# Kernel optimization log

Measured on AMD Instinct MI355X. Metric: run time of the kernel, lower is better.

## Reference

```python
import jax, jax.numpy as jnp
import numpy as np

NUM_CLASSES = 20
NUM_ANCHORS = 3
STRIDES = (8, 16, 32)
FMP = (320, 160, 80)
TOPK = 100
CONF_THRESH = 0.01
NMS_THRESH = 0.5
ANCHOR_SIZE = np.array([[12, 16], [19, 36], [40, 28], [36, 75], [76, 55], [72, 146],
                        [142, 110], [192, 243], [459, 401]], dtype=np.float32).reshape(3, NUM_ANCHORS, 2)


def make_anchors(level):
    h = w = FMP[level]
    ys, xs = jnp.meshgrid(jnp.arange(h, dtype=jnp.float32), jnp.arange(w, dtype=jnp.float32), indexing='ij')
    xy = jnp.stack([xs, ys], axis=-1).reshape(-1, 1, 2) + 0.5            # [HW,1,2] grid centers
    xy = jnp.broadcast_to(xy, (h * w, NUM_ANCHORS, 2))
    wh = jnp.broadcast_to(jnp.asarray(ANCHOR_SIZE[level]), (h * w, NUM_ANCHORS, 2))
    return jnp.concatenate([xy, wh], axis=-1).reshape(-1, 4)             # [HW*A, 4]


def level_topk(obj, cls, reg, level):
    C = NUM_CLASSES
    # [1, ch, H, W] -> [H*W*A, ch_per_anchor], matching permute(1,2,0).view(-1, .)
    obj = obj[0].transpose(1, 2, 0).reshape(-1, 1)
    cls = cls[0].transpose(1, 2, 0).reshape(-1, C)
    reg = reg[0].transpose(1, 2, 0).reshape(-1, 4)
    anchors = make_anchors(level)
    # decode: ctr = (sigmoid(txy)*3 - 1.5 + grid) * stride ; wh = exp(twh) * anchor_wh
    ctr = (jax.nn.sigmoid(reg[:, :2]) * 3.0 - 1.5 + anchors[:, :2]) * STRIDES[level]
    wh = jnp.exp(reg[:, 2:]) * anchors[:, 2:]
    boxes = jnp.concatenate([ctr - 0.5 * wh, ctr + 0.5 * wh], axis=-1)   # [N, 4] xyxy
    scores = (jax.nn.sigmoid(obj) * jax.nn.sigmoid(cls)).reshape(-1)     # [N*C]
    top_s, top_i = jax.lax.top_k(scores, TOPK)
    anchor_idx = top_i // C
    labels = top_i % C
    return top_s, labels, boxes[anchor_idx], top_s > CONF_THRESH


def nms_fixed(boxes, scores, labels, valid):
    # class-aware greedy NMS on a fixed candidate set; suppressed entries get score 0 / keep False
    K = scores.shape[0]
    order = jnp.argsort(-scores)
    b, s, l, v = boxes[order], scores[order], labels[order], valid[order]
    areas = (b[:, 2] - b[:, 0]) * (b[:, 3] - b[:, 1])
    xx1 = jnp.maximum(b[:, None, 0], b[None, :, 0])
    yy1 = jnp.maximum(b[:, None, 1], b[None, :, 1])
    xx2 = jnp.minimum(b[:, None, 2], b[None, :, 2])
    yy2 = jnp.minimum(b[:, None, 3], b[None, :, 3])
    inter = jnp.maximum(1e-10, xx2 - xx1) * jnp.maximum(1e-10, yy2 - yy1)
    iou = inter / (areas[:, None] + areas[None, :] - inter)
    sup_mat = (iou > NMS_THRESH) & (l[:, None] == l[None, :])            # per-class suppression
    idx = jnp.arange(K)

    def body(i, state):
        suppressed, keep = state
        is_kept = jnp.logical_and(jnp.logical_not(suppressed[i]), v[i])
        keep = keep.at[i].set(is_kept)
        suppressed = suppressed | (is_kept & sup_mat[i] & (idx > i))
        return suppressed, keep

    _, keep = jax.lax.fori_loop(0, K, body, (jnp.zeros(K, bool), jnp.zeros(K, bool)))
    return b, s * keep.astype(s.dtype), l, keep


def setup_inputs() -> dict:
    key = jax.random.key(0)
    ks = jax.random.split(key, 9)
    shapes = {
        'obj0': (1, NUM_ANCHORS, 320, 320), 'cls0': (1, NUM_ANCHORS * NUM_CLASSES, 320, 320), 'reg0': (1, NUM_ANCHORS * 4, 320, 320),
        'obj1': (1, NUM_ANCHORS, 160, 160), 'cls1': (1, NUM_ANCHORS * NUM_CLASSES, 160, 160), 'reg1': (1, NUM_ANCHORS * 4, 160, 160),
        'obj2': (1, NUM_ANCHORS, 80, 80), 'cls2': (1, NUM_ANCHORS * NUM_CLASSES, 80, 80), 'reg2': (1, NUM_ANCHORS * 4, 80, 80),
    }
    return {name: jax.random.normal(k, shp, dtype=jnp.float32)
            for k, (name, shp) in zip(ks, shapes.items())}


def reference(obj0, cls0, reg0, obj1, cls1, reg1, obj2, cls2, reg2):
    levels = [(obj0, cls0, reg0), (obj1, cls1, reg1), (obj2, cls2, reg2)]
    parts = [level_topk(o, c, r, i) for i, (o, c, r) in enumerate(levels)]
    scores = jnp.concatenate([p[0] for p in parts])
    labels = jnp.concatenate([p[1] for p in parts])
    boxes = jnp.concatenate([p[2] for p in parts])
    valid = jnp.concatenate([p[3] for p in parts])
    return nms_fixed(boxes, scores, labels, valid)  # (bboxes[300,4], scores[300], labels[300], keep[300])
```

## Files before the change

kernel.cpp:

```cpp
#include <hip/hip_runtime.h>
#include <stdint.h>

typedef unsigned int u32;
typedef unsigned long long u64;

#define TOPK 100
#define CAP 4096
#define NB 512
#define BINBASE 32000u
#define KAB_BLOCKS 788

__device__ const float ANC[3][3][2] = {
  {{12.f,16.f},{19.f,36.f},{40.f,28.f}},
  {{36.f,75.f},{76.f,55.f},{72.f,146.f}},
  {{142.f,110.f},{192.f,243.f},{459.f,401.f}}
};

__device__ __forceinline__ float sigmoidf_(float x) {
  if (x >= 0.f) return 1.f / (1.f + expf(-x));
  float e = expf(x);
  return e / (1.f + e);
}

__device__ __forceinline__ float fcomp2(const float2& v, int q) {
  return q ? v.y : v.x;
}

__global__ __launch_bounds__(256) void kA_scan(
    const float* __restrict__ obj0, const float* __restrict__ cls0,
    const float* __restrict__ obj1, const float* __restrict__ cls1,
    const float* __restrict__ obj2, const float* __restrict__ cls2,
    u32* __restrict__ hist, float* __restrict__ amax)
{
  __shared__ u32 h[NB];
  int tid = threadIdx.x;
  h[tid] = 0; h[tid + 256] = 0;
  __syncthreads();

  int b = blockIdx.x;
  const float *obj, *cls; int P, L, abase; u32 task;
  if (b < 600)      { L=0; obj=obj0; cls=cls0; P=102400; abase=0;      task=(u32)(b*256+tid); }
  else if (b < 750) { L=1; obj=obj1; cls=cls1; P=25600;  abase=307200; task=(u32)((b-600)*256+tid); }
  else              { L=2; obj=obj2; cls=cls2; P=6400;   abase=384000; task=(u32)((b-750)*256+tid); }
  int tpa = P >> 1;
  bool valid = task < (u32)(3*tpa);

  if (valid) {
    int a = (int)(task / (u32)tpa), rem = (int)(task % (u32)tpa);
    int p0 = rem * 2;
    float2 o2 = *(const float2*)(obj + a*P + p0);
    const float* cp = cls + (size_t)(a*20)*P + p0;
    float2 cv[20];
    #pragma unroll
    for (int k = 0; k < 20; ++k) cv[k] = *(const float2*)(cp + (size_t)k*P);
    float2 cm = cv[0];
    #pragma unroll
    for (int k = 1; k < 20; ++k) {
      cm.x = fmaxf(cm.x, cv[k].x); cm.y = fmaxf(cm.y, cv[k].y);
    }
    float2 am2;
    am2.x = sigmoidf_(o2.x) * sigmoidf_(cm.x);
    am2.y = sigmoidf_(o2.y) * sigmoidf_(cm.y);
    *(float2*)(amax + abase + a*P + p0) = am2;
    #pragma unroll
    for (int q = 0; q < 2; ++q) {
      u32 bt = __float_as_uint(fcomp2(am2, q));
      if (bt >= (BINBASE << 15)) {
        u32 bin = (bt >> 15) - BINBASE;
        if (bin < NB) atomicAdd(&h[bin], 1u);
      }
    }
  }
  __syncthreads();
  if (h[tid])       atomicAdd(&hist[L*NB + tid],       h[tid]);
  if (h[tid + 256]) atomicAdd(&hist[L*NB + tid + 256], h[tid + 256]);
}

__global__ __launch_bounds__(256) void kB_collect(
    const float* __restrict__ obj0, const float* __restrict__ cls0,
    const float* __restrict__ obj1, const float* __restrict__ cls1,
    const float* __restrict__ obj2, const float* __restrict__ cls2,
    const float* __restrict__ amax, const u32* __restrict__ hist,
    u32* __restrict__ cnt, u64* __restrict__ cand)
{
  __shared__ u32 s[NB];
  __shared__ u32 sThr;
  int tid = threadIdx.x;
  int b = blockIdx.x;
  const float *obj, *cls; int P, L, abase; u32 task;
  if (b < 600)      { L=0; obj=obj0; cls=cls0; P=102400; abase=0;      task=(u32)(b*256+tid); }
  else if (b < 750) { L=1; obj=obj1; cls=cls1; P=25600;  abase=307200; task=(u32)((b-600)*256+tid); }
  else              { L=2; obj=obj2; cls=cls2; P=6400;   abase=384000; task=(u32)((b-750)*256+tid); }
  int tpa = P >> 1;
  bool valid = task < (u32)(3*tpa);

  s[tid] = hist[L*NB + tid]; s[tid + 256] = hist[L*NB + tid + 256];
  __syncthreads();
  for (int off = 1; off < NB; off <<= 1) {
    u32 v0 = s[tid]       + ((tid + off < NB)       ? s[tid + off]       : 0u);
    u32 v1 = s[tid + 256] + ((tid + 256 + off < NB) ? s[tid + 256 + off] : 0u);
    __syncthreads();
    s[tid] = v0; s[tid + 256] = v1;
    __syncthreads();
  }
  if (tid == 0 && s[0] < TOPK) sThr = BINBASE << 15;
  {
    int i0 = tid, i1 = tid + 256;
    u32 a0 = s[i0], n0 = (i0 + 1 < NB) ? s[i0 + 1] : 0u;
    if (a0 >= TOPK && n0 < TOPK) sThr = (BINBASE + (u32)i0) << 15;
    u32 a1 = s[i1], n1 = (i1 + 1 < NB) ? s[i1 + 1] : 0u;
    if (a1 >= TOPK && n1 < TOPK) sThr = (BINBASE + (u32)i1) << 15;
  }
  __syncthreads();
  u32 thr = sThr;

  if (valid) {
    int a = (int)(task / (u32)tpa), rem = (int)(task % (u32)tpa);
    int p0 = rem * 2;
    float2 am2 = *(const float2*)(amax + abase + a*P + p0);
    bool any = (__float_as_uint(am2.x) >= thr) | (__float_as_uint(am2.y) >= thr);
    if (any) {
      float2 o2 = *(const float2*)(obj + a*P + p0);
      const float* cp = cls + (size_t)(a*20)*P + p0;
      float2 cv[20];
      #pragma unroll
      for (int k = 0; k < 20; ++k) cv[k] = *(const float2*)(cp + (size_t)k*P);
      #pragma unroll
      for (int q = 0; q < 2; ++q) {
        if (__float_as_uint(fcomp2(am2, q)) >= thr) {
          float so = sigmoidf_(fcomp2(o2, q));
          int p = p0 + q;
          #pragma unroll
          for (int k = 0; k < 20; ++k) {
            float sc = so * sigmoidf_(fcomp2(cv[k], q));
            u32 bits = __float_as_uint(sc);
            if (bits >= thr) {
              u32 pos = atomicAdd(&cnt[L], 1u);
              u32 idx = (u32)(p*60 + a*20 + k);
              if (pos < CAP) cand[L*CAP + pos] = ((u64)bits << 32) | (u64)(0x00FFFFFFu - idx);
            }
          }
        }
      }
    }
  }
}

__global__ __launch_bounds__(1024) void kT_select_nms(
    const float* __restrict__ reg0, const float* __restrict__ reg1, const float* __restrict__ reg2,
    const u64* __restrict__ cand, const u32* __restrict__ cnt,
    u64* __restrict__ matg, u32* __restrict__ bar,
    float* __restrict__ out)
{
  extern __shared__ uint8_t smem[];
  u64*    mat   = (u64*)(smem);
  float4* ibox4 = (float4*)(smem + 12000);
  float2* iml2  = (float2*)(smem + 16800);
  float*  x1s   = (float*)(smem + 19200);
  float*  y1s   = (float*)(smem + 20400);
  float*  x2s   = (float*)(smem + 21600);
  float*  y2s   = (float*)(smem + 22800);
  float*  sc2   = (float*)(smem + 24000);
  int*    lb2   = (int*)(smem + 25200);
  int*    vd2   = (int*)(smem + 26400);
  u64*    rowAny= (u64*)(smem + 27600);
  u64*    km    = (u64*)(smem + 27648);
  float*  ars   = (float*)(smem + 27696);
  u64*    sel   = (u64*)(smem + 32800);
  float*  bxs   = (float*)(smem + 35200);
  float*  scs   = (float*)(smem + 40000);
  int*    lbs   = (int*)(smem + 41200);
  int*    vds   = (int*)(smem + 42400);

  int tid = threadIdx.x;
  int b = blockIdx.x;
  if (tid < 300) sel[tid] = 0ull;
  __syncthreads();

  {
    int gL    = (tid >= 768) ? 2 : (tid >= 384) ? 1 : 0;
    int gbase = (gL == 2) ? 768 : (gL == 1) ? 384 : 0;
    int lt    = tid - gbase;
    int gsz   = (gL == 2) ? 256 : 384;

    u32 n = cnt[gL]; if (n > CAP) n = CAP;
    bool useLds = (n <= 496);
    u64* kc = mat + gL*500;
    const u64* cb = cand + gL*CAP;
    u32 n4 = (n + 3u) & ~3u;

    if (useLds) {
      for (u32 j = (u32)lt; j < n; j += gsz) kc[j] = cb[j];
      if (lt < 4 && n + (u32)lt < n4) kc[n + lt] = 0ull;
    }
    __syncthreads();

    if (useLds) {
      for (u32 j = (u32)lt; j < n; j += gsz) {
        u64 kk = kc[j]; int r = 0;
        for (u32 t = 0; t < n4; t += 4) {
          u64 k0 = kc[t], k1 = kc[t+1], k2 = kc[t+2], k3 = kc[t+3];
          r += (k0 > kk) ? 1 : 0; r += (k1 > kk) ? 1 : 0;
          r += (k2 > kk) ? 1 : 0; r += (k3 > kk) ? 1 : 0;
        }
        if (r < TOPK) sel[gL*TOPK + r] = kk;
      }
    } else {
      u32 nn = n & ~3u;
      for (u32 j = (u32)lt; j < n; j += gsz) {
        u64 kk = cb[j]; int r = 0;
        for (u32 t = 0; t < nn; t += 4) {
          r += (cb[t]   > kk) ? 1 : 0; r += (cb[t+1] > kk) ? 1 : 0;
          r += (cb[t+2] > kk) ? 1 : 0; r += (cb[t+3] > kk) ? 1 : 0;
        }
        for (u32 t = nn; t < n; ++t) r += (cb[t] > kk) ? 1 : 0;
        if (r < TOPK) sel[gL*TOPK + r] = kk;
      }
    }
  }
  __syncthreads();

  if (tid < 300) {
    int Lq = tid / TOPK;
    const float* reg; int Pq, W, stride;
    if (Lq == 0)      { reg = reg0; Pq = 102400; W = 320; stride = 8; }
    else if (Lq == 1) { reg = reg1; Pq = 25600;  W = 160; stride = 16; }
    else              { reg = reg2; Pq = 6400;   W = 80;  stride = 32; }
    u64 key = sel[tid];
    if (key == 0) {
      scs[tid] = 0.f; lbs[tid] = 0; vds[tid] = 0;
      bxs[tid*4+0] = bxs[tid*4+1] = bxs[tid*4+2] = bxs[tid*4+3] = 0.f;
    } else {
      float score = __uint_as_float((u32)(key >> 32));
      u32 i = 0x00FFFFFFu - (u32)(key & 0xFFFFFFFFull);
      int c = (int)(i % 60u), p = (int)(i / 60u);
      int aa = c / 20, k = c % 20;
      int x = p % W, y = p / W;
      float tx = reg[(aa*4+0)*Pq + p], ty = reg[(aa*4+1)*Pq + p];
      float tw = reg[(aa*4+2)*Pq + p], th = reg[(aa*4+3)*Pq + p];
      float cx = (sigmoidf_(tx)*3.f - 1.5f + (float)x + 0.5f) * (float)stride;
      float cy = (sigmoidf_(ty)*3.f - 1.5f + (float)y + 0.5f) * (float)stride;
      float bw = expf(tw) * ANC[Lq][aa][0];
      float bh = expf(th) * ANC[Lq][aa][1];
      scs[tid] = score; lbs[tid] = k; vds[tid] = (score > 0.01f) ? 1 : 0;
      bxs[tid*4+0] = cx - 0.5f*bw; bxs[tid*4+1] = cy - 0.5f*bh;
      bxs[tid*4+2] = cx + 0.5f*bw; bxs[tid*4+3] = cy + 0.5f*bh;
    }
  }
  __syncthreads();

  if (tid < 300) {
    int Lm = tid / TOPK, rr = tid % TOPK;
    u64 kk = sel[tid];
    int rank = rr;
    #pragma unroll
    for (int Lo = 0; Lo < 3; ++Lo) {
      if (Lo == Lm) continue;
      const u64* arr = sel + Lo*TOPK;
      bool ge = (Lo < Lm);
      int lo = 0;
      #pragma unroll
      for (int st = 64; st > 0; st >>= 1) {
        int nxt = lo + st;
        if (nxt <= TOPK) {
          u64 v = arr[nxt - 1];
          bool pred = ge ? (v >= kk) : (v > kk);
          if (pred) lo = nxt;
        }
      }
      rank += lo;
    }
    float x1 = bxs[tid*4+0], y1 = bxs[tid*4+1], x2 = bxs[tid*4+2], y2 = bxs[tid*4+3];
    float ar = (x2 - x1) * (y2 - y1);
    ibox4[rank] = make_float4(x1, y1, x2, y2);
    iml2[rank]  = make_float2(ar, (float)lbs[tid]);
    x1s[rank] = x1; y1s[rank] = y1; x2s[rank] = x2; y2s[rank] = y2; ars[rank] = ar;
    sc2[rank] = scs[tid]; lb2[rank] = lbs[tid]; vd2[rank] = vds[tid];
  }
  __syncthreads();

  {
    int w = (b == 0) ? 4 : (b - 1);
    int wave = tid >> 6, lane = tid & 63;
    int j = w*64 + lane;
    bool jv = j < 300;
    float jx1=0.f, jy1=0.f, jx2=0.f, jy2=0.f, jar=0.f; float jlb=-1.f;
    if (jv) { jx1=x1s[j]; jy1=y1s[j]; jx2=x2s[j]; jy2=y2s[j]; jar=ars[j]; jlb=(float)lb2[j]; }
    int ilim = (w+1)*64; if (ilim > 300) ilim = 300;
    for (int i = wave; i < ilim; i += 16) {
      float4 B = ibox4[i];
      float2 M = iml2[i];
      float xx1 = fmaxf(B.x, jx1), yy1 = fmaxf(B.y, jy1);
      float xx2 = fminf(B.z, jx2), yy2 = fminf(B.w, jy2);
      float inter = fmaxf(1e-10f, xx2-xx1) * fmaxf(1e-10f, yy2-yy1);
      float iou = inter / (M.x + jar - inter);
      bool pred = jv && (iou > 0.5f) && (M.y == jlb);
      u64 m = __ballot(pred);
      if (lane == 0) {
        if (b == 0) mat[i*5 + 4] = m;
        else __hip_atomic_store(&matg[i*5 + w], m, __ATOMIC_RELAXED, __HIP_MEMORY_SCOPE_AGENT);
      }
    }
  }
  __syncthreads();

  if (b != 0) {
    if (tid == 0)
      __hip_atomic_fetch_add(bar, 1u, __ATOMIC_RELEASE, __HIP_MEMORY_SCOPE_AGENT);
    return;
  }

  if (tid == 0) {
    while (__hip_atomic_load(bar, __ATOMIC_ACQUIRE, __HIP_MEMORY_SCOPE_AGENT) < 4u)
      __builtin_amdgcn_s_sleep(1);
  }
  __syncthreads();
  for (int idx = tid; idx < 1200; idx += 1024) {
    int w2 = idx / 300, i = idx % 300;
    if (i < (w2+1)*64)
      mat[i*5 + w2] = __hip_atomic_load(&matg[i*5 + w2], __ATOMIC_RELAXED, __HIP_MEMORY_SCOPE_AGENT);
  }
  __syncthreads();

  {
    bool flag = false;
    if (tid < 300) {
      int c = tid >> 6, bq = tid & 63;
      u64 acc = mat[tid*5 + c] & ((bq == 63) ? 0ull : (~0ull << (bq + 1)));
      for (int w = c + 1; w < 5; ++w) acc |= mat[tid*5 + w];
      flag = (acc != 0ull);
    }
    u64 bal = __ballot(flag);
    if ((tid & 63) == 0 && (tid >> 6) < 5) rowAny[tid >> 6] = bal;
  }
  __syncthreads();

  if (tid < 64) {
    int lane = tid;
    u64 vm[5];
    #pragma unroll
    for (int c = 0; c < 5; ++c) {
      int j = c*64 + lane;
      vm[c] = __ballot((j < 300) && (vd2[j] != 0));
    }
    u64 ra[5];
    #pragma unroll
    for (int c = 0; c < 5; ++c) ra[c] = rowAny[c];
    u64 S[5] = {0,0,0,0,0};
    #pragma unroll
    for (int c = 0; c < 5; ++c) {
      u64 kbits = 0;
      int lim = (c == 4) ? 44 : 64;
      for (int t = 0; t < lim; ++t) {
        u64 kept = ((~(S[c] >> t)) & (vm[c] >> t)) & 1ull;
        kbits |= kept << t;
        if (kept & ((ra[c] >> t) & 1ull)) {
          int i = c*64 + t;
          #pragma unroll
          for (int w = 0; w < 5; ++w)
            if (w >= c) S[w] |= mat[i*5 + w];
        }
      }
      if (lane == 0) km[c] = kbits;
    }
  }
  __syncthreads();

  if (tid < 300) {
    float kf = (float)((km[tid >> 6] >> (tid & 63)) & 1ull);
    float4 bq = ibox4[tid];
    out[tid*4+0] = bq.x; out[tid*4+1] = bq.y;
    out[tid*4+2] = bq.z; out[tid*4+3] = bq.w;
    out[1200+tid] = sc2[tid] * kf;
    out[1500+tid] = (float)lb2[tid];
    out[1800+tid] = kf;
  }
}

extern "C" void kernel_launch(void* const* d_in, const int* in_sizes, int n_in,
                              void* d_out, int out_size, void* d_ws, size_t ws_size,
                              hipStream_t stream) {
  const float* obj0 = (const float*)d_in[0];
  const float* cls0 = (const float*)d_in[1];
  const float* reg0 = (const float*)d_in[2];
  const float* obj1 = (const float*)d_in[3];
  const float* cls1 = (const float*)d_in[4];
  const float* reg1 = (const float*)d_in[5];
  const float* obj2 = (const float*)d_in[6];
  const float* cls2 = (const float*)d_in[7];
  const float* reg2 = (const float*)d_in[8];
  float* out = (float*)d_out;

  uint8_t* ws = (uint8_t*)d_ws;
  u32*   hist = (u32*)(ws + 0);
  u32*   cnt  = (u32*)(ws + 6144);
  u32*   bar  = (u32*)(ws + 6156);
  u64*   cand = (u64*)(ws + 8192);
  u64*   matg = (u64*)(ws + 106496);
  float* amax = (float*)(ws + 118496);

  (void)hipMemsetAsync(ws, 0, 6160, stream);

  kA_scan<<<dim3(KAB_BLOCKS), dim3(256), 0, stream>>>(
      obj0, cls0, obj1, cls1, obj2, cls2, hist, amax);
  kB_collect<<<dim3(KAB_BLOCKS), dim3(256), 0, stream>>>(
      obj0, cls0, obj1, cls1, obj2, cls2, amax, hist, cnt, cand);
  kT_select_nms<<<dim3(5), dim3(1024), 43600, stream>>>(
      reg0, reg1, reg2, cand, cnt, matg, bar, out);
}
```

Baseline: 146.2 us.

## Fuse collect and select/NMS kernels via last-blocks-done completion counter

Merges the candidate-collection kernel and the top-k select/NMS kernel into one launch. Blocks are widened to 1024 threads, and a global done counter lets the last five blocks to finish collection take the NMS roles, after spinning until all blocks have arrived. This removes one kernel launch and the inter-kernel gap, but it relies on all blocks being co-resident or finishing so the spin-wait cannot deadlock. It also raises LDS per block to 43.6 KB for every collection block, which may reduce occupancy in the collect phase.

After: 155.7 us. 1.06x slower.

```diff
diff --git a/kernel.cpp b/kernel.cpp
--- a/kernel.cpp
+++ b/kernel.cpp
@@ -8,7 +8,9 @@
 #define CAP 4096
 #define NB 512
 #define BINBASE 32000u
-#define KAB_BLOCKS 788
+#define KA_BLOCKS 788
+#define KBT_BLOCKS 198
+#define FIN_BASE (KBT_BLOCKS - 5)
 
 __device__ const float ANC[3][3][2] = {
   {{12.f,16.f},{19.f,36.f},{40.f,28.f}},
@@ -76,40 +78,62 @@
   if (h[tid + 256]) atomicAdd(&hist[L*NB + tid + 256], h[tid + 256]);
 }
 
-__global__ __launch_bounds__(256) void kB_collect(
+__global__ __launch_bounds__(1024) void kBT_collect_nms(
     const float* __restrict__ obj0, const float* __restrict__ cls0,
     const float* __restrict__ obj1, const float* __restrict__ cls1,
     const float* __restrict__ obj2, const float* __restrict__ cls2,
+    const float* __restrict__ reg0, const float* __restrict__ reg1, const float* __restrict__ reg2,
     const float* __restrict__ amax, const u32* __restrict__ hist,
-    u32* __restrict__ cnt, u64* __restrict__ cand)
+    u32* __restrict__ cnt, u64* __restrict__ cand,
+    u32* __restrict__ done, u32* __restrict__ bar, u64* __restrict__ matg,
+    float* __restrict__ out)
 {
-  __shared__ u32 s[NB];
+  extern __shared__ uint8_t smem[];
+  u32*    s     = (u32*)(smem);
+  u64*    mat   = (u64*)(smem);
+  float4* ibox4 = (float4*)(smem + 12000);
+  float2* iml2  = (float2*)(smem + 16800);
+  float*  x1s   = (float*)(smem + 19200);
+  float*  y1s   = (float*)(smem + 20400);
+  float*  x2s   = (float*)(smem + 21600);
+  float*  y2s   = (float*)(smem + 22800);
+  float*  sc2   = (float*)(smem + 24000);
+  int*    lb2   = (int*)(smem + 25200);
+  int*    vd2   = (int*)(smem + 26400);
+  u64*    rowAny= (u64*)(smem + 27600);
+  u64*    km    = (u64*)(smem + 27648);
+  float*  ars   = (float*)(smem + 27696);
+  u64*    sel   = (u64*)(smem + 32800);
+  float*  bxs   = (float*)(smem + 35200);
+  float*  scs   = (float*)(smem + 40000);
+  int*    lbs   = (int*)(smem + 41200);
+  int*    vds   = (int*)(smem + 42400);
   __shared__ u32 sThr;
+  __shared__ u32 sOld;
+
   int tid = threadIdx.x;
   int b = blockIdx.x;
+
   const float *obj, *cls; int P, L, abase; u32 task;
-  if (b < 600)      { L=0; obj=obj0; cls=cls0; P=102400; abase=0;      task=(u32)(b*256+tid); }
-  else if (b < 750) { L=1; obj=obj1; cls=cls1; P=25600;  abase=307200; task=(u32)((b-600)*256+tid); }
-  else              { L=2; obj=obj2; cls=cls2; P=6400;   abase=384000; task=(u32)((b-750)*256+tid); }
+  if (b < 150)      { L=0; obj=obj0; cls=cls0; P=102400; abase=0;      task=(u32)(b*1024+tid); }
+  else if (b < 188) { L=1; obj=obj1; cls=cls1; P=25600;  abase=307200; task=(u32)((b-150)*1024+tid); }
+  else              { L=2; obj=obj2; cls=cls2; P=6400;   abase=384000; task=(u32)((b-188)*1024+tid); }
   int tpa = P >> 1;
   bool valid = task < (u32)(3*tpa);
 
-  s[tid] = hist[L*NB + tid]; s[tid + 256] = hist[L*NB + tid + 256];
+  if (tid < NB) s[tid] = hist[L*NB + tid];
   __syncthreads();
   for (int off = 1; off < NB; off <<= 1) {
-    u32 v0 = s[tid]       + ((tid + off < NB)       ? s[tid + off]       : 0u);
-    u32 v1 = s[tid + 256] + ((tid + 256 + off < NB) ? s[tid + 256 + off] : 0u);
+    u32 v = 0;
+    if (tid < NB) v = s[tid] + ((tid + off < NB) ? s[tid + off] : 0u);
     __syncthreads();
-    s[tid] = v0; s[tid + 256] = v1;
+    if (tid < NB) s[tid] = v;
     __syncthreads();
   }
   if (tid == 0 && s[0] < TOPK) sThr = BINBASE << 15;
-  {
-    int i0 = tid, i1 = tid + 256;
-    u32 a0 = s[i0], n0 = (i0 + 1 < NB) ? s[i0 + 1] : 0u;
-    if (a0 >= TOPK && n0 < TOPK) sThr = (BINBASE + (u32)i0) << 15;
-    u32 a1 = s[i1], n1 = (i1 + 1 < NB) ? s[i1 + 1] : 0u;
-    if (a1 >= TOPK && n1 < TOPK) sThr = (BINBASE + (u32)i1) << 15;
+  if (tid < NB) {
+    u32 a0 = s[tid], n0 = (tid + 1 < NB) ? s[tid + 1] : 0u;
+    if (a0 >= TOPK && n0 < TOPK) sThr = (BINBASE + (u32)tid) << 15;
   }
   __syncthreads();
   u32 thr = sThr;
@@ -137,43 +161,30 @@
             if (bits >= thr) {
               u32 pos = atomicAdd(&cnt[L], 1u);
               u32 idx = (u32)(p*60 + a*20 + k);
-              if (pos < CAP) cand[L*CAP + pos] = ((u64)bits << 32) | (u64)(0x00FFFFFFu - idx);
+              if (pos < CAP)
+                __hip_atomic_store(&cand[L*CAP + pos],
+                                   ((u64)bits << 32) | (u64)(0x00FFFFFFu - idx),
+                                   __ATOMIC_RELAXED, __HIP_MEMORY_SCOPE_AGENT);
             }
           }
         }
       }
     }
   }
-}
-
-__global__ __launch_bounds__(1024) void kT_select_nms(
-    const float* __restrict__ reg0, const float* __restrict__ reg1, const float* __restrict__ reg2,
-    const u64* __restrict__ cand, const u32* __restrict__ cnt,
-    u64* __restrict__ matg, u32* __restrict__ bar,
-    float* __restrict__ out)
-{
-  extern __shared__ uint8_t smem[];
-  u64*    mat   = (u64*)(smem);
-  float4* ibox4 = (float4*)(smem + 12000);
-  float2* iml2  = (float2*)(smem + 16800);
-  float*  x1s   = (float*)(smem + 19200);
-  float*  y1s   = (float*)(smem + 20400);
-  float*  x2s   = (float*)(smem + 21600);
-  float*  y2s   = (float*)(smem + 22800);
-  float*  sc2   = (float*)(smem + 24000);
-  int*    lb2   = (int*)(smem + 25200);
-  int*    vd2   = (int*)(smem + 26400);
-  u64*    rowAny= (u64*)(smem + 27600);
-  u64*    km    = (u64*)(smem + 27648);
-  float*  ars   = (float*)(smem + 27696);
-  u64*    sel   = (u64*)(smem + 32800);
-  float*  bxs   = (float*)(smem + 35200);
-  float*  scs   = (float*)(smem + 40000);
-  int*    lbs   = (int*)(smem + 41200);
-  int*    vds   = (int*)(smem + 42400);
-
-  int tid = threadIdx.x;
-  int b = blockIdx.x;
+  __syncthreads();
+
+  if (tid == 0) sOld = __hip_atomic_fetch_add(done, 1u, __ATOMIC_ACQ_REL, __HIP_MEMORY_SCOPE_AGENT);
+  __syncthreads();
+  u32 old = sOld;
+  if (old < FIN_BASE) return;
+  int role = (int)(old - FIN_BASE);
+
+  if (tid == 0) {
+    while (__hip_atomic_load(done, __ATOMIC_ACQUIRE, __HIP_MEMORY_SCOPE_AGENT) < (u32)KBT_BLOCKS)
+      __builtin_amdgcn_s_sleep(1);
+  }
+  __syncthreads();
+
   if (tid < 300) sel[tid] = 0ull;
   __syncthreads();
 
@@ -183,14 +194,16 @@
     int lt    = tid - gbase;
     int gsz   = (gL == 2) ? 256 : 384;
 
-    u32 n = cnt[gL]; if (n > CAP) n = CAP;
+    u32 n = __hip_atomic_load(&cnt[gL], __ATOMIC_RELAXED, __HIP_MEMORY_SCOPE_AGENT);
+    if (n > CAP) n = CAP;
     bool useLds = (n <= 496);
     u64* kc = mat + gL*500;
     const u64* cb = cand + gL*CAP;
     u32 n4 = (n + 3u) & ~3u;
 
     if (useLds) {
-      for (u32 j = (u32)lt; j < n; j += gsz) kc[j] = cb[j];
+      for (u32 j = (u32)lt; j < n; j += gsz)
+        kc[j] = __hip_atomic_load(&cb[j], __ATOMIC_RELAXED, __HIP_MEMORY_SCOPE_AGENT);
       if (lt < 4 && n + (u32)lt < n4) kc[n + lt] = 0ull;
     }
     __syncthreads();
@@ -206,14 +219,11 @@
         if (r < TOPK) sel[gL*TOPK + r] = kk;
       }
     } else {
-      u32 nn = n & ~3u;
       for (u32 j = (u32)lt; j < n; j += gsz) {
-        u64 kk = cb[j]; int r = 0;
-        for (u32 t = 0; t < nn; t += 4) {
-          r += (cb[t]   > kk) ? 1 : 0; r += (cb[t+1] > kk) ? 1 : 0;
-          r += (cb[t+2] > kk) ? 1 : 0; r += (cb[t+3] > kk) ? 1 : 0;
-        }
-        for (u32 t = nn; t < n; ++t) r += (cb[t] > kk) ? 1 : 0;
+        u64 kk = __hip_atomic_load(&cb[j], __ATOMIC_RELAXED, __HIP_MEMORY_SCOPE_AGENT);
+        int r = 0;
+        for (u32 t = 0; t < n; ++t)
+          r += (__hip_atomic_load(&cb[t], __ATOMIC_RELAXED, __HIP_MEMORY_SCOPE_AGENT) > kk) ? 1 : 0;
         if (r < TOPK) sel[gL*TOPK + r] = kk;
       }
     }
@@ -280,7 +290,7 @@
   __syncthreads();
 
   {
-    int w = (b == 0) ? 4 : (b - 1);
+    int w = (role == 4) ? 4 : role;
     int wave = tid >> 6, lane = tid & 63;
     int j = w*64 + lane;
     bool jv = j < 300;
@@ -297,14 +307,14 @@
       bool pred = jv && (iou > 0.5f) && (M.y == jlb);
       u64 m = __ballot(pred);
       if (lane == 0) {
-        if (b == 0) mat[i*5 + 4] = m;
+        if (role == 4) mat[i*5 + 4] = m;
         else __hip_atomic_store(&matg[i*5 + w], m, __ATOMIC_RELAXED, __HIP_MEMORY_SCOPE_AGENT);
       }
     }
   }
   __syncthreads();
 
-  if (b != 0) {
+  if (role != 4) {
     if (tid == 0)
       __hip_atomic_fetch_add(bar, 1u, __ATOMIC_RELEASE, __HIP_MEMORY_SCOPE_AGENT);
     return;
@@ -394,17 +404,17 @@
   uint8_t* ws = (uint8_t*)d_ws;
   u32*   hist = (u32*)(ws + 0);
   u32*   cnt  = (u32*)(ws + 6144);
-  u32*   bar  = (u32*)(ws + 6156);
+  u32*   done = (u32*)(ws + 6156);
+  u32*   bar  = (u32*)(ws + 6160);
   u64*   cand = (u64*)(ws + 8192);
   u64*   matg = (u64*)(ws + 106496);
   float* amax = (float*)(ws + 118496);
 
-  (void)hipMemsetAsync(ws, 0, 6160, stream);
-
-  kA_scan<<<dim3(KAB_BLOCKS), dim3(256), 0, stream>>>(
+  (void)hipMemsetAsync(ws, 0, 6164, stream);
+
+  kA_scan<<<dim3(KA_BLOCKS), dim3(256), 0, stream>>>(
       obj0, cls0, obj1, cls1, obj2, cls2, hist, amax);
-  kB_collect<<<dim3(KAB_BLOCKS), dim3(256), 0, stream>>>(
-      obj0, cls0, obj1, cls1, obj2, cls2, amax, hist, cnt, cand);
-  kT_select_nms<<<dim3(5), dim3(1024), 43600, stream>>>(
-      reg0, reg1, reg2, cand, cnt, matg, bar, out);
+  kBT_collect_nms<<<dim3(KBT_BLOCKS), dim3(1024), 43600, stream>>>(
+      obj0, cls0, obj1, cls1, obj2, cls2, reg0, reg1, reg2,
+      amax, hist, cnt, cand, done, bar, matg, out);
 }
```
